# Performance work log

Hardware: AMD Instinct MI355X
Metric: run time of the kernel (lower is better)

## Reference

```python
import jax, jax.numpy as jnp
import numpy as np

E = 2048      # embed_size
H = 16        # heads_size
D_HEAD = E // H          # 128
D_ROPE = 32
SPLIT = D_HEAD - D_ROPE  # 96
C = 512       # d_kv_comp
B, S = 2, 2048
ROT_SCALE = 40.0


def _rotary_emb(seq_len):
    # inv_freq has d_rope//4 entries; emb is [S, d_rope//2]
    half = D_ROPE // 2
    inv_freq = 1.0 / (10000.0 ** (jnp.arange(0, half, 2, dtype=jnp.float32) / half))
    t = jnp.arange(seq_len, dtype=jnp.float32) / ROT_SCALE
    freqs = jnp.einsum('i,j->ij', t, inv_freq)
    return jnp.concatenate([freqs, freqs], axis=-1)  # [S, d_rope//2]


def _rotate_half(x):
    x1, x2 = jnp.split(x, 2, axis=-1)
    return jnp.concatenate([-x2, x1], axis=-1)


def _apply_rotary(x, cos, sin):
    rd = cos.shape[-1]
    x_rot, x_base = x[..., :rd], x[..., rd:]
    x_rot = x_rot * cos + _rotate_half(x_rot) * sin
    return jnp.concatenate([x_rot, x_base], axis=-1)


def setup_inputs() -> dict:
    key = jax.random.key(0)
    ks = jax.random.split(key, 10)

    def xav(k, shape):
        fan_in, fan_out = shape
        lim = float(np.sqrt(6.0 / (fan_in + fan_out)))
        return jax.random.uniform(k, shape, jnp.float32, -lim, lim)

    return {
        'h': jax.random.normal(ks[0], (B, S, E), jnp.float32),
        'W_dkv': xav(ks[1], (E, C)), 'b_dkv': jnp.zeros((C,), jnp.float32),
        'W_dq':  xav(ks[2], (E, C)), 'b_dq':  jnp.zeros((C,), jnp.float32),
        'W_uk':  xav(ks[3], (C, H * SPLIT)),  'b_uk': jnp.zeros((H * SPLIT,), jnp.float32),
        'W_uv':  xav(ks[4], (C, H * D_HEAD)), 'b_uv': jnp.zeros((H * D_HEAD,), jnp.float32),
        'W_uq':  xav(ks[5], (C, H * SPLIT)),  'b_uq': jnp.zeros((H * SPLIT,), jnp.float32),
        'W_qr':  xav(ks[6], (C, H * D_ROPE)), 'b_qr': jnp.zeros((H * D_ROPE,), jnp.float32),
        'W_kr':  xav(ks[7], (E, H * D_ROPE)), 'b_kr': jnp.zeros((H * D_ROPE,), jnp.float32),
        'W_out': xav(ks[8], (H * D_HEAD, E)), 'b_out': jnp.zeros((E,), jnp.float32),
    }


def reference(h, W_dkv, b_dkv, W_dq, b_dq, W_uk, b_uk, W_uv, b_uv,
              W_uq, b_uq, W_qr, b_qr, W_kr, b_kr, W_out, b_out):
    Bq, Sq, _ = h.shape
    c_kv = h @ W_dkv + b_dkv                                   # [B,S,C]
    k = (c_kv @ W_uk + b_uk).reshape(Bq, Sq, H, SPLIT)
    v = (c_kv @ W_uv + b_uv).reshape(Bq, Sq, H, D_HEAD)
    c_q = h @ W_dq + b_dq
    q_base = (c_q @ W_uq + b_uq).reshape(Bq, Sq, H, SPLIT)
    q_rot = (c_q @ W_qr + b_qr).reshape(Bq, Sq, H, D_ROPE)

    emb = _rotary_emb(Sq)                                      # [S, d_rope//2]
    cos = jnp.cos(emb)[None, :, None, :]
    sin = jnp.sin(emb)[None, :, None, :]
    q_rot = _apply_rotary(q_rot, cos, sin)
    k_rot = _apply_rotary((h @ W_kr + b_kr).reshape(Bq, Sq, H, D_ROPE), cos, sin)

    q = jnp.concatenate([q_base, q_rot], axis=-1)              # [B,S,H,d_head]
    k_full = jnp.concatenate([k, k_rot], axis=-1)

    scores = jnp.einsum('bqhd,bkhd->bhqk', q, k_full) / jnp.sqrt(jnp.float32(D_HEAD))
    causal = jnp.tril(jnp.ones((Sq, Sq), dtype=bool))
    scores = jnp.where(causal[None, None], scores, -jnp.inf)
    attn = jax.nn.softmax(scores, axis=-1)
    out = jnp.einsum('bhqk,bkhd->bqhd', attn, v).reshape(Bq, Sq, H * D_HEAD)
    out = out @ W_out + b_out
    return out, c_kv, k_rot
```

## Files before the change

kernel.cpp:

```cpp
#include <hip/hip_runtime.h>
#include <hip/hip_bf16.h>

#define B_   2
#define S_   2048
#define E_   2048
#define H_   16
#define DH_  128
#define DR_  32
#define SP_  96
#define C_   512
#define M_   (B_ * S_)

#define LOG2E 1.4426950408889634f

typedef __attribute__((ext_vector_type(8))) short short8;
typedef __attribute__((ext_vector_type(4))) float floatx4;

__device__ __forceinline__ float bfu(unsigned short u) {
  return __uint_as_float((unsigned)u << 16);
}
__device__ __forceinline__ unsigned short f2bf(float f) {
  unsigned u = __float_as_uint(f);
  return (unsigned short)((u + 0x7fff + ((u >> 16) & 1)) >> 16);
}

__device__ __forceinline__ void gload16(const void* g, void* l) {
  __builtin_amdgcn_global_load_lds(
      (const __attribute__((address_space(1))) void*)g,
      (__attribute__((address_space(3))) void*)l, 16, 0, 0);
}

struct TEnt { const float* W; unsigned short* Wt; int K, N, ntiles, nx; };
struct TTab { TEnt e[8]; };

__global__ __launch_bounds__(256) void prep_kernel(
    const float* __restrict__ hsrc, unsigned short* __restrict__ hdst,
    TTab tab) {
  if (blockIdx.x < 8192) {
    size_t i = ((size_t)blockIdx.x * 256 + threadIdx.x) * 4;
    float4 v = *(const float4*)(hsrc + i);
    ushort4 w;
    w.x = f2bf(v.x); w.y = f2bf(v.y); w.z = f2bf(v.z); w.w = f2bf(v.w);
    *(ushort4*)(hdst + i) = w;
    return;
  }
  __shared__ unsigned short T[32][33];
  int rem = blockIdx.x - 8192;
  const float* W = nullptr; unsigned short* Wt = nullptr;
  int K = 0, N = 0, nx = 1;
  bool done = false;
#pragma unroll
  for (int j = 0; j < 8; j++) {
    if (!done) {
      if (rem < tab.e[j].ntiles) {
        W = tab.e[j].W; Wt = tab.e[j].Wt;
        K = tab.e[j].K; N = tab.e[j].N; nx = tab.e[j].nx;
        done = true;
      } else {
        rem -= tab.e[j].ntiles;
      }
    }
  }
  int n0 = (rem % nx) * 32, k0 = (rem / nx) * 32;
  int t = threadIdx.x, lane = t & 31, grp = t >> 5;
#pragma unroll
  for (int p = 0; p < 4; p++) {
    int k = p * 8 + grp;
    T[lane][k] = f2bf(W[(size_t)(k0 + k) * N + n0 + lane]);
  }
  __syncthreads();
#pragma unroll
  for (int p = 0; p < 4; p++) {
    int n = p * 8 + grp;
    Wt[(size_t)(n0 + n) * K + k0 + lane] = T[n][lane];
  }
}

struct Seg {
  float* outF;
  unsigned short* outB;
  const float* bias;
  const float* biasM;
  float* krotF;
  int orow, chunk, gstride, obase, nstart, ileave, rope;
  float oscale;
};

__device__ __forceinline__ void gemm_body(
    const unsigned short* __restrict__ A, const unsigned short* __restrict__ W,
    int K, int bm, int bn, const Seg& sg) {
  __shared__ unsigned short As0[128 * 32];
  __shared__ unsigned short Bs0[128 * 32];
  __shared__ unsigned short As1[128 * 32];
  __shared__ unsigned short Bs1[128 * 32];
  int tid = threadIdx.x;
  int lane = tid & 63, wave = tid >> 6;
  int l16 = lane & 15, quad = lane >> 4;
  int wm = (wave & 3) * 32, wn = (wave >> 2) * 64;

  floatx4 acc[2][4];
#pragma unroll
  for (int mt = 0; mt < 2; mt++)
#pragma unroll
    for (int nt = 0; nt < 4; nt++) acc[mt][nt] = (floatx4){0.f, 0.f, 0.f, 0.f};

  int srow = lane >> 2, scol = (lane & 3) * 8;
  const unsigned short* Ag = A + (size_t)(bm + wave * 16 + srow) * K + scol;
  const unsigned short* Bg = W + (size_t)(bn + wave * 16 + srow) * K + scol;
  int lo = wave * 512;

#define GSTAGE(kk, Asb, Bsb) do {      \
    gload16(Ag + (kk), &Asb[lo]);      \
    gload16(Bg + (kk), &Bsb[lo]); } while (0)

#define GCOMPUTE(Asb, Bsb) do {                                            \
    short8 af[2], bfv[4];                                                  \
    _Pragma("unroll")                                                      \
    for (int mt = 0; mt < 2; mt++)                                         \
      af[mt] = *(const short8*)&Asb[(wm + mt * 16 + l16) * 32 + quad * 8]; \
    _Pragma("unroll")                                                      \
    for (int nt = 0; nt < 4; nt++)                                         \
      bfv[nt] = *(const short8*)&Bsb[(wn + nt * 16 + l16) * 32 + quad * 8];\
    _Pragma("unroll")                                                      \
    for (int mt = 0; mt < 2; mt++)                                         \
      _Pragma("unroll")                                                    \
      for (int nt = 0; nt < 4; nt++)                                       \
        acc[mt][nt] = __builtin_amdgcn_mfma_f32_16x16x32_bf16(             \
            af[mt], bfv[nt], acc[mt][nt], 0, 0, 0); } while (0)

  GSTAGE(0, As0, Bs0);
  __syncthreads();
  for (int k0 = 0; k0 < K; k0 += 64) {
    GSTAGE(k0 + 32, As1, Bs1);
    GCOMPUTE(As0, Bs0);
    __syncthreads();
    if (k0 + 64 < K) GSTAGE(k0 + 64, As0, Bs0);
    GCOMPUTE(As1, Bs1);
    __syncthreads();
  }
#undef GSTAGE
#undef GCOMPUTE

#pragma unroll
  for (int mt = 0; mt < 2; mt++) {
    int m0 = bm + wm + mt * 16 + quad * 4;
    float bm4[4] = {0.f, 0.f, 0.f, 0.f};
    if (sg.biasM) {
#pragma unroll
      for (int r = 0; r < 4; r++) bm4[r] = sg.biasM[m0 + r];
    }
#pragma unroll
    for (int nt = 0; nt < 4; nt++) {
      int n = bn + wn + nt * 16 + l16;
      int nl = n - sg.nstart;
      float bv = sg.biasM ? 0.f : sg.bias[nl];
      int ncol = sg.obase + (nl / sg.chunk) * sg.gstride + (nl % sg.chunk);
      if (sg.ileave)
        ncol = (ncol & ~31) | ((ncol & 15) << 1) | ((ncol >> 4) & 1);
      bool rot_half = sg.rope && ((nl & 31) < 16);
#pragma unroll
      for (int r = 0; r < 4; r++) {
        float val = (acc[mt][nt][r] + (sg.biasM ? bm4[r] : bv)) * sg.oscale;
        if (rot_half) {
          int j = l16 & 7;
          int srw = (m0 + r) & (S_ - 1);
          float ang = ((float)srw / 40.0f) *
                      exp2f(-1.6609640474436813f * (float)j);
          float cc = cosf(ang), ss = sinf(ang);
          float part = __shfl_xor(val, 8);
          val = (l16 < 8) ? (val * cc - part * ss) : (val * cc + part * ss);
        }
        if (sg.rope == 1 && sg.krotF)
          sg.krotF[(size_t)(m0 + r) * (H_ * DR_) + nl] = val;
        size_t idx = (size_t)(m0 + r) * sg.orow + ncol;
        if (sg.outF) sg.outF[idx] = val;
        if (sg.outB) sg.outB[idx] = f2bf(val);
      }
    }
  }
}

__global__ __launch_bounds__(512) void mfma_gemm(
    const unsigned short* __restrict__ A, const unsigned short* __restrict__ Wt,
    Seg s0, Seg s1, Seg s2, int K) {
  int gx = gridDim.x;
  int nwg = gx * gridDim.y;
  int flat = blockIdx.y * gx + blockIdx.x;
  int w = (flat & 7) * (nwg >> 3) + (flat >> 3);
  int by = w / gx, bx = w - by * gx;
  int bm = by * 128, bn = bx * 128;
  Seg sg = (bn >= s2.nstart) ? s2 : ((bn >= s1.nstart) ? s1 : s0);
  gemm_body(A, Wt, K, bm, bn, sg);
}

__global__ __launch_bounds__(512) void fused_gemm3(
    const unsigned short* __restrict__ ckv, const unsigned short* __restrict__ cq,
    const unsigned short* __restrict__ wuk, const unsigned short* __restrict__ wuv,
    const unsigned short* __restrict__ wuq,
    unsigned short* __restrict__ kbf, unsigned short* __restrict__ vtbf,
    unsigned short* __restrict__ qbf,
    const float* __restrict__ b_uk, const float* __restrict__ b_uv,
    const float* __restrict__ b_uq, const float* __restrict__ b_qr,
    float qscale) {
  int flat = blockIdx.x;
  int w = (flat & 7) * 176 + (flat >> 3);
  const unsigned short* A; const unsigned short* W;
  int bm, bn;
  Seg sg;
  sg.outF = nullptr; sg.oscale = 1.f; sg.ileave = 0; sg.nstart = 0;
  sg.rope = 0; sg.krotF = nullptr;
  if (w < 384) {
    int by = w / 12, bx = w - by * 12;
    bm = by * 128; bn = bx * 128;
    A = ckv; W = wuk;
    sg.outB = kbf; sg.bias = b_uk; sg.biasM = nullptr;
    sg.orow = 2048; sg.chunk = SP_; sg.gstride = DH_; sg.obase = 0;
  } else if (w < 896) {
    int w2 = w - 384;
    int by = w2 >> 5, bx = w2 & 31;
    bm = by * 128; bn = bx * 128;
    A = wuv; W = ckv;
    sg.outB = vtbf; sg.bias = nullptr; sg.biasM = b_uv;
    sg.orow = M_; sg.chunk = M_; sg.gstride = M_; sg.obase = 0; sg.ileave = 1;
  } else {
    int w3 = w - 896;
    int by = w3 >> 4, bx = w3 & 15;
    bm = by * 128; bn = bx * 128;
    A = cq; W = wuq;
    sg.outB = qbf; sg.biasM = nullptr; sg.orow = 2048; sg.oscale = qscale;
    if (bn >= 1536) {
      sg.bias = b_qr; sg.chunk = DR_; sg.gstride = DH_; sg.obase = SP_;
      sg.nstart = 1536; sg.rope = 2;
    } else {
      sg.bias = b_uq; sg.chunk = SP_; sg.gstride = DH_; sg.obase = 0;
    }
  }
  gemm_body(A, W, 512, bm, bn, sg);
}

#define PST 72
__global__ __launch_bounds__(256, 2) void attn_kernel(
    const unsigned short* __restrict__ qf, const unsigned short* __restrict__ kf,
    const unsigned short* __restrict__ vt, unsigned short* __restrict__ ao) {
  __shared__ unsigned short Ks[2][64 * 128];
  __shared__ unsigned short Vs[2][128 * 64];
  __shared__ unsigned short Ps[4][16 * PST];

  int bid0 = blockIdx.x;
  int xcd  = bid0 & 7;
  int idx  = bid0 >> 3;
  int r_   = idx >> 5;
  int q_   = idx & 31;
  int bh   = xcd * 4 + (q_ >> 3);
  int jp   = r_ ? (15 - (q_ & 7)) : (q_ & 7);
  int h    = bh & 15;
  int b    = bh >> 4;
  int jjh  = 31 - jp;
  int jjl  = jp;
  int q0h  = jjh << 6, q0l = jjl << 6;
  int nchunks = jjh + 1;

  int tid  = threadIdx.x;
  int wave = tid >> 6;
  int lane = tid & 63;
  int l16  = lane & 15;
  int quad = lane >> 4;
  int x7   = l16 & 7;

  int krow = tid >> 2;
  int kst  = (tid & 3) * 4;
  int vrow = tid >> 1;
  int vst  = (tid & 1) * 4;
  const unsigned short* kg =
      kf + ((size_t)(b * S_ + krow)) * 2048 + h * 128 + kst * 8;
  const unsigned short* vg =
      vt + ((size_t)(h * 128 + vrow)) * 4096 + b * 2048 + vst * 8;
  int kwl[4], vwl[4];
#pragma unroll
  for (int i = 0; i < 4; i++) {
    kwl[i] = krow * 128 + (((kst + i) ^ (krow & 7)) * 8);
    vwl[i] = vrow * 64  + (((vst + i) ^ (vrow & 7)) * 8);
  }

  short8 qfh[4], qfl[4];
  {
    const unsigned short* qb =
        qf + ((size_t)(b * S_ + q0h + wave * 16 + l16)) * 2048 + h * 128 + quad * 8;
#pragma unroll
    for (int c = 0; c < 4; c++) qfh[c] = *(const short8*)(qb + c * 32);
  }
  {
    const unsigned short* qb =
        qf + ((size_t)(b * S_ + q0l + wave * 16 + l16)) * 2048 + h * 128 + quad * 8;
#pragma unroll
    for (int c = 0; c < 4; c++) qfl[c] = *(const short8*)(qb + c * 32);
  }

  floatx4 OaccH[8], OaccL[8];
#pragma unroll
  for (int dt = 0; dt < 8; dt++) {
    OaccH[dt] = (floatx4){0.f, 0.f, 0.f, 0.f};
    OaccL[dt] = (floatx4){0.f, 0.f, 0.f, 0.f};
  }
  float lpH[4] = {0.f, 0.f, 0.f, 0.f};
  float lpL[4] = {0.f, 0.f, 0.f, 0.f};
  int qgh = q0h + wave * 16;
  int qgl = q0l + wave * 16;

#define SCOMPUTE(QF, OC, LP, QG, DIAG) do {                                   \
    const unsigned short* Kc = Ks[cur];                                       \
    const unsigned short* Vc = Vs[cur];                                       \
    floatx4 sv[4];                                                            \
    _Pragma("unroll")                                                         \
    for (int nt = 0; nt < 4; nt++) sv[nt] = (floatx4){0.f, 0.f, 0.f, 0.f};    \
    __builtin_amdgcn_s_setprio(1);                                            \
    _Pragma("unroll")                                                         \
    for (int nt = 0; nt < 4; nt++)                                            \
      _Pragma("unroll")                                                       \
      for (int c = 0; c < 4; c++) {                                           \
        short8 kfr = *(const short8*)&Kc[(nt * 16 + l16) * 128 +              \
                                         ((4 * c + quad) ^ x7) * 8];          \
        sv[nt] = __builtin_amdgcn_mfma_f32_16x16x32_bf16(QF[c], kfr, sv[nt],  \
                                                         0, 0, 0);            \
      }                                                                       \
    __builtin_amdgcn_s_setprio(0);                                            \
    unsigned short* P = Ps[wave];                                             \
    _Pragma("unroll")                                                         \
    for (int ks = 0; ks < 2; ks++)                                            \
      _Pragma("unroll")                                                       \
      for (int r = 0; r < 4; r++) {                                           \
        float p0 = exp2f(fminf(sv[2 * ks][r], 80.f));                         \
        float p1 = exp2f(fminf(sv[2 * ks + 1][r], 80.f));                     \
        if (DIAG) {                                                           \
          int q_r = QG + quad * 4 + r;                                        \
          int kc0 = kt0 + ks * 32 + l16;                                      \
          if (kc0 > q_r)      p0 = 0.f;                                       \
          if (kc0 + 16 > q_r) p1 = 0.f;                                       \
        }                                                                     \
        unsigned pk;                                                          \
        asm("v_cvt_pk_bf16_f32 %0, %1, %2" : "=v"(pk) : "v"(p0), "v"(p1));    \
        *(unsigned*)&P[(quad * 4 + r) * PST + ks * 32 + 2 * l16] = pk;        \
        LP[r] += p0 + p1;                                                     \
      }                                                                       \
    short8 pf0 = *(const short8*)&P[l16 * PST + quad * 8];                    \
    short8 pf1 = *(const short8*)&P[l16 * PST + 32 + quad * 8];               \
    __builtin_amdgcn_s_setprio(1);                                            \
    _Pragma("unroll")                                                         \
    for (int dt = 0; dt < 8; dt++) {                                          \
      short8 vf0 = *(const short8*)&Vc[(dt * 16 + l16) * 64 +                 \
                                       ((quad) ^ x7) * 8];                    \
      OC[dt] = __builtin_amdgcn_mfma_f32_16x16x32_bf16(pf0, vf0, OC[dt],      \
                                                       0, 0, 0);              \
      short8 vf1 = *(const short8*)&Vc[(dt * 16 + l16) * 64 +                 \
                                       ((4 + quad) ^ x7) * 8];                \
      OC[dt] = __builtin_amdgcn_mfma_f32_16x16x32_bf16(pf1, vf1, OC[dt],      \
                                                       0, 0, 0);              \
    }                                                                         \
    __builtin_amdgcn_s_setprio(0);                                            \
  } while (0)

  short8 kr[4], vr[4];
#pragma unroll
  for (int i = 0; i < 4; i++) {
    kr[i] = *(const short8*)(kg + i * 8);
    vr[i] = *(const short8*)(vg + i * 8);
  }
#pragma unroll
  for (int i = 0; i < 4; i++) {
    *(short8*)&Ks[0][kwl[i]] = kr[i];
    *(short8*)&Vs[0][vwl[i]] = vr[i];
  }
#pragma unroll
  for (int i = 0; i < 4; i++) {
    kr[i] = *(const short8*)(kg + 131072 + i * 8);
    vr[i] = *(const short8*)(vg + 64 + i * 8);
  }
  __syncthreads();

  int cur = 0;
  for (int t = 0; t < nchunks; t++) {
#pragma unroll
    for (int i = 0; i < 4; i++) {
      *(short8*)&Ks[cur ^ 1][kwl[i]] = kr[i];
      *(short8*)&Vs[cur ^ 1][vwl[i]] = vr[i];
    }
    {
      int tf = (t + 2 < nchunks) ? t + 2 : nchunks - 1;
      const unsigned short* ksrc = kg + (size_t)tf * 131072;
      const unsigned short* vsrc = vg + tf * 64;
#pragma unroll
      for (int i = 0; i < 4; i++) {
        kr[i] = *(const short8*)(ksrc + i * 8);
        vr[i] = *(const short8*)(vsrc + i * 8);
      }
    }
    int kt0 = t << 6;
    SCOMPUTE(qfh, OaccH, lpH, qgh, (t == jjh));
    if (t <= jjl) SCOMPUTE(qfl, OaccL, lpL, qgl, (t == jjl));
    __syncthreads();
    cur ^= 1;
  }
#undef SCOMPUTE

#pragma unroll
  for (int side = 0; side < 2; side++) {
    floatx4* OC = side ? OaccL : OaccH;
    float*   LP = side ? lpL : lpH;
    int qg = (side ? qgl : qgh) + quad * 4;
    float linv[4];
#pragma unroll
    for (int r = 0; r < 4; r++) {
      float ls = LP[r];
#pragma unroll
      for (int sh = 1; sh < 16; sh <<= 1) ls += __shfl_xor(ls, sh);
      linv[r] = 1.0f / ls;
    }
#pragma unroll
    for (int r = 0; r < 4; r++) {
      unsigned short* dst =
          ao + ((size_t)(b * S_ + qg + r)) * 2048 + h * 128 + l16;
#pragma unroll
      for (int dt = 0; dt < 8; dt++) dst[dt * 16] = f2bf(OC[dt][r] * linv[r]);
    }
  }
}

static inline Seg mkseg(float* oF, unsigned short* oB, const float* bias,
                        const float* biasM, int orow, int chunk, int gstride,
                        int obase, int nstart, int ileave, float oscale,
                        int rope, float* krotF) {
  Seg s;
  s.outF = oF; s.outB = oB; s.bias = bias; s.biasM = biasM; s.krotF = krotF;
  s.orow = orow; s.chunk = chunk; s.gstride = gstride;
  s.obase = obase; s.nstart = nstart; s.ileave = ileave; s.rope = rope;
  s.oscale = oscale;
  return s;
}
static inline Seg segnone() {
  return mkseg(nullptr, nullptr, nullptr, nullptr, 1, 1, 1, 0, 0x7fffffff,
               0, 1.f, 0, nullptr);
}
static inline TEnt mktent(const float* W, unsigned short* Wt, int K, int N,
                          int ntiles, int nx) {
  TEnt e;
  e.W = W; e.Wt = Wt; e.K = K; e.N = N; e.ntiles = ntiles; e.nx = nx;
  return e;
}

extern "C" void kernel_launch(void* const* d_in, const int* in_sizes, int n_in,
                              void* d_out, int out_size, void* d_ws, size_t ws_size,
                              hipStream_t stream) {
  const float* h     = (const float*)d_in[0];
  const float* W_dkv = (const float*)d_in[1];
  const float* b_dkv = (const float*)d_in[2];
  const float* W_dq  = (const float*)d_in[3];
  const float* b_dq  = (const float*)d_in[4];
  const float* W_uk  = (const float*)d_in[5];
  const float* b_uk  = (const float*)d_in[6];
  const float* W_uv  = (const float*)d_in[7];
  const float* b_uv  = (const float*)d_in[8];
  const float* W_uq  = (const float*)d_in[9];
  const float* b_uq  = (const float*)d_in[10];
  const float* W_qr  = (const float*)d_in[11];
  const float* b_qr  = (const float*)d_in[12];
  const float* W_kr  = (const float*)d_in[13];
  const float* b_kr  = (const float*)d_in[14];
  const float* W_out = (const float*)d_in[15];
  const float* b_out = (const float*)d_in[16];

  float* out      = (float*)d_out;
  float* out_ckv  = out + (size_t)M_ * E_;
  float* out_krot = out_ckv + (size_t)M_ * C_;

  unsigned short* w16 = (unsigned short*)d_ws;
  unsigned short* h_bf   = w16;
  unsigned short* q_bf   = w16 + 8388608;
  unsigned short* k_bf   = w16 + 16777216;
  unsigned short* vt_bf  = w16 + 25165824;
  unsigned short* ao_bf  = w16 + 33554432;
  unsigned short* ckv_bf = w16 + 41943040;
  unsigned short* cq_bf  = w16 + 44040192;
  unsigned short* Wt_dkv = w16 + 46137344;
  unsigned short* Wt_dq  = w16 + 47185920;
  unsigned short* Wt_kr  = w16 + 48234496;
  unsigned short* Wt_uk  = w16 + 49283072;
  unsigned short* Wt_uv  = w16 + 50069504;
  unsigned short* Wt_uq  = w16 + 51118080;
  unsigned short* Wt_qr  = w16 + 51904512;
  unsigned short* Wt_out = w16 + 52166656;
  (void)Wt_qr;

  dim3 blk256(256), blk512(512);
  const float qscale = 0.08838834764831845f * LOG2E;

  TTab tab;
  tab.e[0] = mktent(W_dkv, Wt_dkv, E_, C_,       1024, 16);
  tab.e[1] = mktent(W_dq,  Wt_dq,  E_, C_,       1024, 16);
  tab.e[2] = mktent(W_kr,  Wt_kr,  E_, H_ * DR_, 1024, 16);
  tab.e[3] = mktent(W_uk,  Wt_uk,  C_, H_ * SP_,  768, 48);
  tab.e[4] = mktent(W_uv,  Wt_uv,  C_, H_ * DH_, 1024, 64);
  tab.e[5] = mktent(W_uq,  Wt_uq,  C_, H_ * SP_,  768, 48);
  tab.e[6] = mktent(W_qr,  w16 + 51904512, C_, H_ * DR_,  256, 16);
  tab.e[7] = mktent(W_out, Wt_out, E_, E_,       4096, 64);
  prep_kernel<<<18176, blk256, 0, stream>>>(h, h_bf, tab);

  mfma_gemm<<<dim3(1536 / 128, M_ / 128), blk512, 0, stream>>>(
      h_bf, Wt_dkv,
      mkseg(out_ckv, ckv_bf, b_dkv, nullptr, C_, C_, C_, 0, 0, 0, 1.f, 0, nullptr),
      mkseg(nullptr, cq_bf,  b_dq,  nullptr, C_, C_, C_, 0, 512, 0, 1.f, 0, nullptr),
      mkseg(nullptr, k_bf,   b_kr,  nullptr, 2048, DR_, DH_, SP_, 1024, 0, 1.f,
            1, out_krot),
      E_);

  fused_gemm3<<<1408, blk512, 0, stream>>>(
      ckv_bf, cq_bf, Wt_uk, Wt_uv, Wt_uq, k_bf, vt_bf, q_bf,
      b_uk, b_uv, b_uq, b_qr, qscale);

  attn_kernel<<<B_ * H_ * 16, blk256, 0, stream>>>(q_bf, k_bf, vt_bf, ao_bf);

  mfma_gemm<<<dim3(E_ / 128, M_ / 128), blk512, 0, stream>>>(
      ao_bf, Wt_out,
      mkseg(out, nullptr, b_out, nullptr, E_, E_, E_, 0, 0, 0, 1.f, 0, nullptr),
      segnone(), segnone(), E_);
}
```

Baseline: 362.9 us.

## Use 4-wave GEMM blocks with 64x64 warp tiles and BK=64 staging

```diff
diff --git a/kernel.cpp b/kernel.cpp
--- a/kernel.cpp
+++ b/kernel.cpp
@@ -86,63 +86,96 @@
   float oscale;
 };
 
+template <bool BK64>
 __device__ __forceinline__ void gemm_body(
     const unsigned short* __restrict__ A, const unsigned short* __restrict__ W,
     int K, int bm, int bn, const Seg& sg) {
-  __shared__ unsigned short As0[128 * 32];
-  __shared__ unsigned short Bs0[128 * 32];
-  __shared__ unsigned short As1[128 * 32];
-  __shared__ unsigned short Bs1[128 * 32];
+  __shared__ unsigned short As0[BK64 ? 128 * 64 : 128 * 32];
+  __shared__ unsigned short Bs0[BK64 ? 128 * 64 : 128 * 32];
+  __shared__ unsigned short As1[BK64 ? 128 * 64 : 128 * 32];
+  __shared__ unsigned short Bs1[BK64 ? 128 * 64 : 128 * 32];
   int tid = threadIdx.x;
   int lane = tid & 63, wave = tid >> 6;
   int l16 = lane & 15, quad = lane >> 4;
-  int wm = (wave & 3) * 32, wn = (wave >> 2) * 64;
-
-  floatx4 acc[2][4];
-#pragma unroll
-  for (int mt = 0; mt < 2; mt++)
+  int wm = (wave & 1) * 64, wn = (wave >> 1) * 64;
+
+  floatx4 acc[4][4];
+#pragma unroll
+  for (int mt = 0; mt < 4; mt++)
 #pragma unroll
     for (int nt = 0; nt < 4; nt++) acc[mt][nt] = (floatx4){0.f, 0.f, 0.f, 0.f};
 
+  int c0 = wave * 2, c1 = c0 + 1;
   int srow = lane >> 2, scol = (lane & 3) * 8;
-  const unsigned short* Ag = A + (size_t)(bm + wave * 16 + srow) * K + scol;
-  const unsigned short* Bg = W + (size_t)(bn + wave * 16 + srow) * K + scol;
-  int lo = wave * 512;
-
-#define GSTAGE(kk, Asb, Bsb) do {      \
-    gload16(Ag + (kk), &Asb[lo]);      \
-    gload16(Bg + (kk), &Bsb[lo]); } while (0)
-
-#define GCOMPUTE(Asb, Bsb) do {                                            \
-    short8 af[2], bfv[4];                                                  \
+  const unsigned short* Ag0 = A + (size_t)(bm + c0 * 16 + srow) * K + scol;
+  const unsigned short* Ag1 = A + (size_t)(bm + c1 * 16 + srow) * K + scol;
+  const unsigned short* Bg0 = W + (size_t)(bn + c0 * 16 + srow) * K + scol;
+  const unsigned short* Bg1 = W + (size_t)(bn + c1 * 16 + srow) * K + scol;
+
+#define GSTAGE(kk, Asb, Bsb) do {            \
+    gload16(Ag0 + (kk), &Asb[c0 * 512]);     \
+    gload16(Ag1 + (kk), &Asb[c1 * 512]);     \
+    gload16(Bg0 + (kk), &Bsb[c0 * 512]);     \
+    gload16(Bg1 + (kk), &Bsb[c1 * 512]); } while (0)
+
+#define GSTAGE64(kk, Asb, Bsb) do {                 \
+    gload16(Ag0 + (kk),      &Asb[c0 * 512]);       \
+    gload16(Ag1 + (kk),      &Asb[c1 * 512]);       \
+    gload16(Bg0 + (kk),      &Bsb[c0 * 512]);       \
+    gload16(Bg1 + (kk),      &Bsb[c1 * 512]);       \
+    gload16(Ag0 + (kk) + 32, &Asb[4096 + c0 * 512]);\
+    gload16(Ag1 + (kk) + 32, &Asb[4096 + c1 * 512]);\
+    gload16(Bg0 + (kk) + 32, &Bsb[4096 + c0 * 512]);\
+    gload16(Bg1 + (kk) + 32, &Bsb[4096 + c1 * 512]); } while (0)
+
+#define GCOMPUTE(Ap, Bp) do {                                              \
+    const unsigned short* Asb = (Ap);                                      \
+    const unsigned short* Bsb = (Bp);                                      \
+    short8 af[4], bfv[4];                                                  \
     _Pragma("unroll")                                                      \
-    for (int mt = 0; mt < 2; mt++)                                         \
+    for (int mt = 0; mt < 4; mt++)                                         \
       af[mt] = *(const short8*)&Asb[(wm + mt * 16 + l16) * 32 + quad * 8]; \
     _Pragma("unroll")                                                      \
     for (int nt = 0; nt < 4; nt++)                                         \
       bfv[nt] = *(const short8*)&Bsb[(wn + nt * 16 + l16) * 32 + quad * 8];\
     _Pragma("unroll")                                                      \
-    for (int mt = 0; mt < 2; mt++)                                         \
+    for (int mt = 0; mt < 4; mt++)                                         \
       _Pragma("unroll")                                                    \
       for (int nt = 0; nt < 4; nt++)                                       \
         acc[mt][nt] = __builtin_amdgcn_mfma_f32_16x16x32_bf16(             \
             af[mt], bfv[nt], acc[mt][nt], 0, 0, 0); } while (0)
 
-  GSTAGE(0, As0, Bs0);
-  __syncthreads();
-  for (int k0 = 0; k0 < K; k0 += 64) {
-    GSTAGE(k0 + 32, As1, Bs1);
-    GCOMPUTE(As0, Bs0);
+  if constexpr (BK64) {
+    GSTAGE64(0, As0, Bs0);
     __syncthreads();
-    if (k0 + 64 < K) GSTAGE(k0 + 64, As0, Bs0);
-    GCOMPUTE(As1, Bs1);
+    for (int k0 = 0; k0 < K; k0 += 128) {
+      GSTAGE64(k0 + 64, As1, Bs1);
+      GCOMPUTE(&As0[0], &Bs0[0]);
+      GCOMPUTE(&As0[4096], &Bs0[4096]);
+      __syncthreads();
+      if (k0 + 128 < K) GSTAGE64(k0 + 128, As0, Bs0);
+      GCOMPUTE(&As1[0], &Bs1[0]);
+      GCOMPUTE(&As1[4096], &Bs1[4096]);
+      __syncthreads();
+    }
+  } else {
+    GSTAGE(0, As0, Bs0);
     __syncthreads();
+    for (int k0 = 0; k0 < K; k0 += 64) {
+      GSTAGE(k0 + 32, As1, Bs1);
+      GCOMPUTE(&As0[0], &Bs0[0]);
+      __syncthreads();
+      if (k0 + 64 < K) GSTAGE(k0 + 64, As0, Bs0);
+      GCOMPUTE(&As1[0], &Bs1[0]);
+      __syncthreads();
+    }
   }
 #undef GSTAGE
+#undef GSTAGE64
 #undef GCOMPUTE
 
 #pragma unroll
-  for (int mt = 0; mt < 2; mt++) {
+  for (int mt = 0; mt < 4; mt++) {
     int m0 = bm + wm + mt * 16 + quad * 4;
     float bm4[4] = {0.f, 0.f, 0.f, 0.f};
     if (sg.biasM) {
@@ -166,7 +199,7 @@
           int srw = (m0 + r) & (S_ - 1);
           float ang = ((float)srw / 40.0f) *
                       exp2f(-1.6609640474436813f * (float)j);
-          float cc = cosf(ang), ss = sinf(ang);
+          float cc = __cosf(ang), ss = __sinf(ang);
           float part = __shfl_xor(val, 8);
           val = (l16 < 8) ? (val * cc - part * ss) : (val * cc + part * ss);
         }
@@ -180,7 +213,8 @@
   }
 }
 
-__global__ __launch_bounds__(512) void mfma_gemm(
+template <bool BK64>
+__global__ __launch_bounds__(256) void mfma_gemm(
     const unsigned short* __restrict__ A, const unsigned short* __restrict__ Wt,
     Seg s0, Seg s1, Seg s2, int K) {
   int gx = gridDim.x;
@@ -190,10 +224,10 @@
   int by = w / gx, bx = w - by * gx;
   int bm = by * 128, bn = bx * 128;
   Seg sg = (bn >= s2.nstart) ? s2 : ((bn >= s1.nstart) ? s1 : s0);
-  gemm_body(A, Wt, K, bm, bn, sg);
-}
-
-__global__ __launch_bounds__(512) void fused_gemm3(
+  gemm_body<BK64>(A, Wt, K, bm, bn, sg);
+}
+
+__global__ __launch_bounds__(256) void fused_gemm3(
     const unsigned short* __restrict__ ckv, const unsigned short* __restrict__ cq,
     const unsigned short* __restrict__ wuk, const unsigned short* __restrict__ wuv,
     const unsigned short* __restrict__ wuq,
@@ -235,7 +269,7 @@
       sg.bias = b_uq; sg.chunk = SP_; sg.gstride = DH_; sg.obase = 0;
     }
   }
-  gemm_body(A, W, 512, bm, bn, sg);
+  gemm_body<false>(A, W, 512, bm, bn, sg);
 }
 
 #define PST 72
@@ -490,7 +524,7 @@
   unsigned short* Wt_out = w16 + 52166656;
   (void)Wt_qr;
 
-  dim3 blk256(256), blk512(512);
+  dim3 blk256(256);
   const float qscale = 0.08838834764831845f * LOG2E;
 
   TTab tab;
@@ -504,7 +538,7 @@
   tab.e[7] = mktent(W_out, Wt_out, E_, E_,       4096, 64);
   prep_kernel<<<18176, blk256, 0, stream>>>(h, h_bf, tab);
 
-  mfma_gemm<<<dim3(1536 / 128, M_ / 128), blk512, 0, stream>>>(
+  mfma_gemm<true><<<dim3(1536 / 128, M_ / 128), blk256, 0, stream>>>(
       h_bf, Wt_dkv,
       mkseg(out_ckv, ckv_bf, b_dkv, nullptr, C_, C_, C_, 0, 0, 0, 1.f, 0, nullptr),
       mkseg(nullptr, cq_bf,  b_dq,  nullptr, C_, C_, C_, 0, 512, 0, 1.f, 0, nullptr),
@@ -512,13 +546,13 @@
             1, out_krot),
       E_);
 
-  fused_gemm3<<<1408, blk512, 0, stream>>>(
+  fused_gemm3<<<1408, blk256, 0, stream>>>(
       ckv_bf, cq_bf, Wt_uk, Wt_uv, Wt_uq, k_bf, vt_bf, q_bf,
       b_uk, b_uv, b_uq, b_qr, qscale);
 
   attn_kernel<<<B_ * H_ * 16, blk256, 0, stream>>>(q_bf, k_bf, vt_bf, ao_bf);
 
-  mfma_gemm<<<dim3(E_ / 128, M_ / 128), blk512, 0, stream>>>(
+  mfma_gemm<true><<<dim3(E_ / 128, M_ / 128), blk256, 0, stream>>>(
       ao_bf, Wt_out,
       mkseg(out, nullptr, b_out, nullptr, E_, E_, E_, 0, 0, 0, 1.f, 0, nullptr),
       segnone(), segnone(), E_);
```

Measured after the change: 343.3 us. 1.06x faster.
